# Kernel optimization log

Measured on AMD Instinct MI355X. Metric: run time of the kernel, lower is better.

## Reference

```python
import jax, jax.numpy as jnp
import numpy as np

B, T, C, H = 4, 2048, 1024, 16
D = C // H  # head_dim = 64


def setup_inputs() -> dict:
    key = jax.random.key(0)
    k1, k2, k3 = jax.random.split(key, 3)
    x = jax.random.normal(k1, (B, T, C), dtype=jnp.float32)
    w_attn = jax.random.normal(k2, (C, 3 * C), dtype=jnp.float32) * (1.0 / np.sqrt(C))
    b_attn = jnp.zeros((3 * C,), dtype=jnp.float32)
    w_proj = jax.random.normal(k3, (C, C), dtype=jnp.float32) * (1.0 / np.sqrt(C))
    b_proj = jnp.zeros((C,), dtype=jnp.float32)
    return {"x": x, "w_attn": w_attn, "b_attn": b_attn, "w_proj": w_proj, "b_proj": b_proj}


def reference(x, w_attn, b_attn, w_proj, b_proj):
    Bx, Tx, Cx = x.shape
    qkv = x @ w_attn + b_attn                      # (B, T, 3C)
    q, k, v = jnp.split(qkv, 3, axis=2)
    # (B, T, C) -> (B, H, T, D)
    q = q.reshape(Bx, Tx, H, D).transpose(0, 2, 1, 3)
    k = k.reshape(Bx, Tx, H, D).transpose(0, 2, 1, 3)
    v = v.reshape(Bx, Tx, H, D).transpose(0, 2, 1, 3)
    scores = jnp.einsum('bhqd,bhkd->bhqk', q, k) / jnp.sqrt(jnp.float32(D))
    causal = jnp.tril(jnp.ones((Tx, Tx), dtype=bool))
    scores = jnp.where(causal[None, None], scores, jnp.float32(-jnp.inf))
    probs = jax.nn.softmax(scores, axis=-1)
    out = jnp.einsum('bhqk,bhkd->bhqd', probs, v)  # (B, H, T, D)
    out = out.transpose(0, 2, 1, 3).reshape(Bx, Tx, Cx)
    return out @ w_proj + b_proj
```

## Files before the change

kernel.cpp:

```cpp
#include <hip/hip_runtime.h>

#define AS1 __attribute__((address_space(1)))
#define AS3 __attribute__((address_space(3)))

using bf16x8  = __attribute__((ext_vector_type(8))) __bf16;
using floatx4 = __attribute__((ext_vector_type(4))) float;

#define SCQ 0.18033688f

__device__ inline ushort f2b(float f) {
    __bf16 h = (__bf16)f;
    return __builtin_bit_cast(ushort, h);
}

__device__ inline float fexp2(float x) {
    float r;
    asm("v_exp_f32 %0, %1" : "=v"(r) : "v"(x));
    return r;
}

__device__ inline unsigned cvtpk_bf16(float lo, float hi) {
    unsigned r;
    asm("v_cvt_pk_bf16_f32 %0, %1, %2" : "=v"(r) : "v"(lo), "v"(hi));
    return r;
}
__device__ inline void plswap32(unsigned& a, unsigned& b) {
    asm("v_permlane32_swap_b32 %0, %1" : "+v"(a), "+v"(b));
}
__device__ inline void plswap16(unsigned& a, unsigned& b) {
    asm("v_permlane16_swap_b32 %0, %1" : "+v"(a), "+v"(b));
}

#define BARRIER_A() asm volatile("s_waitcnt lgkmcnt(0)\n\ts_barrier" ::: "memory")
#define BARRIER_B() asm volatile("s_barrier" ::: "memory")

__device__ inline bf16x8 pack_swap(floatx4 ej0, floatx4 ej1) {
    unsigned x0 = cvtpk_bf16(ej0[0], ej0[1]);
    unsigned x1 = cvtpk_bf16(ej0[2], ej0[3]);
    unsigned y0 = cvtpk_bf16(ej1[0], ej1[1]);
    unsigned y1 = cvtpk_bf16(ej1[2], ej1[3]);
    plswap32(x0, y0); plswap16(x0, y0);
    plswap32(x1, y1); plswap16(x1, y1);
    union { unsigned u[4]; bf16x8 v; } ua;
    ua.u[0] = x0; ua.u[1] = x1; ua.u[2] = y0; ua.u[3] = y1;
    return ua.v;
}

__global__ void k_prep(const float* __restrict__ x, ushort* __restrict__ xb,
                       const float* __restrict__ wa, ushort* __restrict__ waT,
                       const float* __restrict__ wp, ushort* __restrict__ wpT)
{
    __shared__ float tile[32][33];
    int blk = blockIdx.x;
    if (blk < 8192) {
        int i = (blk * 256 + threadIdx.x) * 4;
        float4 v = *(const float4*)(x + i);
        ushort4 o;
        o.x = f2b(v.x); o.y = f2b(v.y); o.z = f2b(v.z); o.w = f2b(v.w);
        *(ushort4*)(xb + i) = o;
        return;
    }
    const float* in; ushort* out; int R, Ncol, bx, by; float scale; int scale_cols;
    if (blk < 11264) {
        int idx = blk - 8192;
        in = wa; out = waT; R = 1024; Ncol = 3072;
        bx = idx % 96; by = idx / 96; scale = SCQ; scale_cols = 1024;
    } else {
        int idx = blk - 11264;
        in = wp; out = wpT; R = 1024; Ncol = 1024;
        bx = idx % 32; by = idx / 32; scale = 1.0f; scale_cols = 0;
    }
    int tx = threadIdx.x & 31, ty = threadIdx.x >> 5;
    int c0 = bx * 32, r0 = by * 32;
    for (int i = 0; i < 32; i += 8)
        tile[ty + i][tx] = in[(size_t)(r0 + ty + i) * Ncol + c0 + tx];
    __syncthreads();
    for (int i = 0; i < 32; i += 8) {
        int n = c0 + ty + i;
        float v = tile[tx][ty + i];
        if (n < scale_cols) v *= scale;
        out[(size_t)n * R + r0 + tx] = f2b(v);
    }
}

__device__ inline void xcd_swizzle(int& bx, int& by) {
    int gx = gridDim.x, lin = blockIdx.x + gx * blockIdx.y;
    int nwg = gx * gridDim.y;
    int swz = (lin & 7) * (nwg >> 3) + (lin >> 3);
    bx = swz % gx; by = swz / gx;
}

__global__ __launch_bounds__(256, 4) void k_gemm_bt(
    const ushort* __restrict__ A, const ushort* __restrict__ Bt,
    const float* __restrict__ bias, float* __restrict__ outv,
    int M, int N, int K)
{
    __shared__ __align__(16) ushort As[128 * 64];
    __shared__ __align__(16) ushort Bs[128 * 64];
    int tid = threadIdx.x;
    int bxs, bys; xcd_swizzle(bxs, bys);
    int m0 = bys * 128, n0 = bxs * 128;
    int lane = tid & 63;
    int wm = (tid >> 7) * 64;
    int wn = ((tid >> 6) & 1) * 64;
    int lr = lane & 15, quad = lane >> 4;

    floatx4 acc[4][4] = {};
    const ushort* ags[4]; const ushort* bgs[4]; int sdst[4];
    #pragma unroll
    for (int it = 0; it < 4; ++it) {
        int slot = tid + 256 * it;
        int row = slot >> 3, ch = slot & 7;
        ags[it] = A  + (size_t)(m0 + row) * K + ch * 8;
        bgs[it] = Bt + (size_t)(n0 + row) * K + ch * 8;
        sdst[it] = slot * 8;
    }

    for (int kt = 0; kt < K; kt += 64) {
        #pragma unroll
        for (int it = 0; it < 4; ++it) {
            __builtin_amdgcn_global_load_lds((const AS1 unsigned int*)(ags[it] + kt),
                                             (AS3 unsigned int*)&As[sdst[it]], 16, 0, 0);
            __builtin_amdgcn_global_load_lds((const AS1 unsigned int*)(bgs[it] + kt),
                                             (AS3 unsigned int*)&Bs[sdst[it]], 16, 0, 0);
        }
        asm volatile("s_waitcnt vmcnt(0)" ::: "memory");
        __syncthreads();
        bf16x8 af[4][2], bf[4][2];
        #pragma unroll
        for (int i = 0; i < 4; ++i) {
            af[i][0] = *(const bf16x8*)&As[(wm + 16 * i + lr) * 64 + quad * 8];
            af[i][1] = *(const bf16x8*)&As[(wm + 16 * i + lr) * 64 + 32 + quad * 8];
        }
        #pragma unroll
        for (int j = 0; j < 4; ++j) {
            bf[j][0] = *(const bf16x8*)&Bs[(wn + 16 * j + lr) * 64 + quad * 8];
            bf[j][1] = *(const bf16x8*)&Bs[(wn + 16 * j + lr) * 64 + 32 + quad * 8];
        }
        #pragma unroll
        for (int i = 0; i < 4; ++i)
            #pragma unroll
            for (int j = 0; j < 4; ++j) {
                acc[i][j] = __builtin_amdgcn_mfma_f32_16x16x32_bf16(af[i][0], bf[j][0], acc[i][j], 0, 0, 0);
                acc[i][j] = __builtin_amdgcn_mfma_f32_16x16x32_bf16(af[i][1], bf[j][1], acc[i][j], 0, 0, 0);
            }
        __syncthreads();
    }

    #pragma unroll
    for (int j = 0; j < 4; ++j) {
        int col = n0 + wn + 16 * j + lr;
        float bv = bias[col];
        #pragma unroll
        for (int i = 0; i < 4; ++i) {
            int row = m0 + wm + 16 * i + quad * 4;
            #pragma unroll
            for (int r = 0; r < 4; ++r)
                outv[(size_t)(row + r) * N + col] = acc[i][j][r] + bv;
        }
    }
}

__global__ __launch_bounds__(256, 4) void k_gemm_qkv(
    const ushort* __restrict__ A, const ushort* __restrict__ Bt,
    const float* __restrict__ bias, ushort* __restrict__ qkv, ushort* __restrict__ vt)
{
    constexpr int K = 1024;
    __shared__ __align__(16) ushort As[128 * 64];
    __shared__ __align__(16) ushort Bs[128 * 64];
    int tid = threadIdx.x;
    int bxs, bys; xcd_swizzle(bxs, bys);
    int m0 = bys * 128, n0 = bxs * 128;
    int lane = tid & 63;
    int wm = (tid >> 7) * 64;
    int wn = ((tid >> 6) & 1) * 64;
    int lr = lane & 15, quad = lane >> 4;

    floatx4 acc[4][4] = {};
    const ushort* ags[4]; const ushort* bgs[4]; int sdst[4];
    #pragma unroll
    for (int it = 0; it < 4; ++it) {
        int slot = tid + 256 * it;
        int row = slot >> 3, ch = slot & 7;
        ags[it] = A  + (size_t)(m0 + row) * K + ch * 8;
        bgs[it] = Bt + (size_t)(n0 + row) * K + ch * 8;
        sdst[it] = slot * 8;
    }

    for (int kt = 0; kt < K; kt += 64) {
        #pragma unroll
        for (int it = 0; it < 4; ++it) {
            __builtin_amdgcn_global_load_lds((const AS1 unsigned int*)(ags[it] + kt),
                                             (AS3 unsigned int*)&As[sdst[it]], 16, 0, 0);
            __builtin_amdgcn_global_load_lds((const AS1 unsigned int*)(bgs[it] + kt),
                                             (AS3 unsigned int*)&Bs[sdst[it]], 16, 0, 0);
        }
        asm volatile("s_waitcnt vmcnt(0)" ::: "memory");
        __syncthreads();
        bf16x8 af[4][2], bf[4][2];
        #pragma unroll
        for (int i = 0; i < 4; ++i) {
            af[i][0] = *(const bf16x8*)&As[(wm + 16 * i + lr) * 64 + quad * 8];
            af[i][1] = *(const bf16x8*)&As[(wm + 16 * i + lr) * 64 + 32 + quad * 8];
        }
        #pragma unroll
        for (int j = 0; j < 4; ++j) {
            bf[j][0] = *(const bf16x8*)&Bs[(wn + 16 * j + lr) * 64 + quad * 8];
            bf[j][1] = *(const bf16x8*)&Bs[(wn + 16 * j + lr) * 64 + 32 + quad * 8];
        }
        #pragma unroll
        for (int i = 0; i < 4; ++i)
            #pragma unroll
            for (int j = 0; j < 4; ++j) {
                acc[i][j] = __builtin_amdgcn_mfma_f32_16x16x32_bf16(af[i][0], bf[j][0], acc[i][j], 0, 0, 0);
                acc[i][j] = __builtin_amdgcn_mfma_f32_16x16x32_bf16(af[i][1], bf[j][1], acc[i][j], 0, 0, 0);
            }
        __syncthreads();
    }

    int bb = m0 >> 11;
    #pragma unroll
    for (int j = 0; j < 4; ++j) {
        int col = n0 + wn + 16 * j + lr;
        float bv = bias[col];
        if (col < 1024) bv *= SCQ;
        if (col < 2048) {
            #pragma unroll
            for (int i = 0; i < 4; ++i) {
                int row = m0 + wm + 16 * i + quad * 4;
                #pragma unroll
                for (int r = 0; r < 4; ++r)
                    qkv[(size_t)(row + r) * 2048 + col] = f2b(acc[i][j][r] + bv);
            }
        } else {
            int h = (col - 2048) >> 6, d = (col - 2048) & 63;
            ushort* vbase = vt + ((size_t)(bb * 16 + h) * 64 + d) * 2048;
            #pragma unroll
            for (int i = 0; i < 4; ++i) {
                int t0 = (m0 + wm + 16 * i + quad * 4) & 2047;
                ushort4 pk;
                ((ushort*)&pk)[0] = f2b(acc[i][j][0] + bv);
                ((ushort*)&pk)[1] = f2b(acc[i][j][1] + bv);
                ((ushort*)&pk)[2] = f2b(acc[i][j][2] + bv);
                ((ushort*)&pk)[3] = f2b(acc[i][j][3] + bv);
                *(ushort4*)&vbase[t0] = pk;
            }
        }
    }
}

__device__ __forceinline__ void attn_tile(
    const ushort* __restrict__ Kb, const ushort* __restrict__ Vb,
    bf16x8 aq0, bf16x8 aq1, bf16x8 ones,
    floatx4 (&o)[4], floatx4& lacc,
    int kt, int ktd, int qrow, int lr, int quad, int c0, int c1)
{
    floatx4 s[4];
    __builtin_amdgcn_s_setprio(1);
    #pragma unroll
    for (int j = 0; j < 4; ++j) {
        const ushort* kr = &Kb[(16 * j + lr) * 64];
        bf16x8 bk0 = *(const bf16x8*)(kr + c0);
        bf16x8 bk1 = *(const bf16x8*)(kr + c1);
        floatx4 z = {};
        s[j] = __builtin_amdgcn_mfma_f32_16x16x32_bf16(bk0, aq0, z, 0, 0, 0);
        s[j] = __builtin_amdgcn_mfma_f32_16x16x32_bf16(bk1, aq1, s[j], 0, 0, 0);
    }
    __builtin_amdgcn_s_setprio(0);
    floatx4 e[4];
    if (kt == ktd) {
        int qa = qrow + lr;
        #pragma unroll
        for (int j = 0; j < 4; ++j)
            #pragma unroll
            for (int r = 0; r < 4; ++r)
                e[j][r] = ((kt * 64 + 16 * j + quad * 4 + r) > qa) ? 0.f : fexp2(s[j][r]);
    } else {
        #pragma unroll
        for (int j = 0; j < 4; ++j)
            #pragma unroll
            for (int r = 0; r < 4; ++r)
                e[j][r] = fexp2(s[j][r]);
    }
    bf16x8 ap0 = pack_swap(e[0], e[1]);
    bf16x8 ap1 = pack_swap(e[2], e[3]);
    __builtin_amdgcn_s_setprio(1);
    lacc = __builtin_amdgcn_mfma_f32_16x16x32_bf16(ap0, ones, lacc, 0, 0, 0);
    lacc = __builtin_amdgcn_mfma_f32_16x16x32_bf16(ap1, ones, lacc, 0, 0, 0);
    #pragma unroll
    for (int jd = 0; jd < 4; ++jd) {
        const ushort* vr = &Vb[(16 * jd + lr) * 64];
        bf16x8 bv0 = *(const bf16x8*)(vr + c0);
        bf16x8 bv1 = *(const bf16x8*)(vr + c1);
        o[jd] = __builtin_amdgcn_mfma_f32_16x16x32_bf16(ap0, bv0, o[jd], 0, 0, 0);
        o[jd] = __builtin_amdgcn_mfma_f32_16x16x32_bf16(ap1, bv1, o[jd], 0, 0, 0);
    }
    __builtin_amdgcn_s_setprio(0);
}

__global__ __launch_bounds__(512, 4) void k_attn(const ushort* __restrict__ qkv,
                                                 const ushort* __restrict__ vt,
                                                 ushort* __restrict__ out)
{
    constexpr int T = 2048, SQK = 2048, C = 1024;
    __shared__ __align__(16) ushort Ks[4][64 * 64];
    __shared__ __align__(16) ushort Vs[4][64 * 64];
    int tid = threadIdx.x;
    int lane = tid & 63, wave = tid >> 6;
    int lr = lane & 15, quad = lane >> 4, lk = quad * 8;

    int lin = blockIdx.x + 8 * blockIdx.y;
    int qt  = lin >> 6;
    int bh  = lin & 63;
    int b = bh >> 4, h = bh & 15;
    size_t base = (size_t)b * T * SQK;
    const ushort* kg0 = qkv + base + 1024 + h * 64;
    const ushort* vg0 = vt + (size_t)bh * 64 * 2048;

    int srow = tid >> 3;
    int sg   = (tid & 7) ^ (srow & 7);
    int sdst = tid * 8;
    const ushort* kgs = kg0 + (size_t)srow * SQK + sg * 8;
    const ushort* vgs = vg0 + (size_t)srow * 2048 + sg * 8;

    bf16x8 ones;
    #pragma unroll
    for (int i = 0; i < 8; ++i) ones[i] = (__bf16)1.0f;
    int c0 = (quad ^ (lr & 7)) * 8;
    int c1 = ((4 + quad) ^ (lr & 7)) * 8;

    int qtA = qt, qtB = 15 - qt;
    int qrowA = qtA * 128 + wave * 16;
    int qrowB = qtB * 128 + wave * 16;
    int ktdA = qrowA >> 6, ktdB = qrowB >> 6;
    const ushort* qpA = qkv + base + (size_t)(qrowA + lr) * SQK + h * 64;
    const ushort* qpB = qkv + base + (size_t)(qrowB + lr) * SQK + h * 64;
    bf16x8 aqA0 = *(const bf16x8*)(qpA + lk);
    bf16x8 aqA1 = *(const bf16x8*)(qpA + 32 + lk);
    bf16x8 aqB0 = *(const bf16x8*)(qpB + lk);
    bf16x8 aqB1 = *(const bf16x8*)(qpB + 32 + lk);
    floatx4 oA[4] = {}, oB[4] = {};
    floatx4 laccA = {}, laccB = {};
    int ktmax = 2 * qtB + 1;

    #pragma unroll
    for (int p = 0; p < 3; ++p) {
        __builtin_amdgcn_global_load_lds((const AS1 unsigned int*)(kgs + (size_t)p * 64 * SQK),
                                         (AS3 unsigned int*)&Ks[p][sdst], 16, 0, 0);
        __builtin_amdgcn_global_load_lds((const AS1 unsigned int*)(vgs + p * 64),
                                         (AS3 unsigned int*)&Vs[p][sdst], 16, 0, 0);
    }

    for (int kt = 0; kt <= ktmax; ++kt) {
        BARRIER_A();
        if (kt + 3 <= ktmax) {
            int bidx = (kt + 3) & 3;
            __builtin_amdgcn_global_load_lds((const AS1 unsigned int*)(kgs + (size_t)(kt + 3) * 64 * SQK),
                                             (AS3 unsigned int*)&Ks[bidx][sdst], 16, 0, 0);
            __builtin_amdgcn_global_load_lds((const AS1 unsigned int*)(vgs + (kt + 3) * 64),
                                             (AS3 unsigned int*)&Vs[bidx][sdst], 16, 0, 0);
            asm volatile("s_waitcnt vmcnt(6)" ::: "memory");
        } else if (kt + 2 <= ktmax) {
            asm volatile("s_waitcnt vmcnt(4)" ::: "memory");
        } else if (kt + 1 <= ktmax) {
            asm volatile("s_waitcnt vmcnt(2)" ::: "memory");
        } else {
            asm volatile("s_waitcnt vmcnt(0)" ::: "memory");
        }
        BARRIER_B();

        const ushort* Kb = Ks[kt & 3];
        const ushort* Vb = Vs[kt & 3];
        if (kt <= ktdB)
            attn_tile(Kb, Vb, aqB0, aqB1, ones, oB, laccB, kt, ktdB, qrowB, lr, quad, c0, c1);
        if (kt <= ktdA)
            attn_tile(Kb, Vb, aqA0, aqA1, ones, oA, laccA, kt, ktdA, qrowA, lr, quad, c0, c1);
    }

    #pragma unroll
    for (int r = 0; r < 4; ++r) {
        float invA = 1.0f / laccA[r];
        float invB = 1.0f / laccB[r];
        int rowA = b * T + qrowA + quad * 4 + r;
        int rowB = b * T + qrowB + quad * 4 + r;
        #pragma unroll
        for (int jd = 0; jd < 4; ++jd) {
            out[(size_t)rowA * C + h * 64 + 16 * jd + lr] = f2b(oA[jd][r] * invA);
            out[(size_t)rowB * C + h * 64 + 16 * jd + lr] = f2b(oB[jd][r] * invB);
        }
    }
}

extern "C" void kernel_launch(void* const* d_in, const int* in_sizes, int n_in,
                              void* d_out, int out_size, void* d_ws, size_t ws_size,
                              hipStream_t stream) {
    const float* x      = (const float*)d_in[0];
    const float* w_attn = (const float*)d_in[1];
    const float* b_attn = (const float*)d_in[2];
    const float* w_proj = (const float*)d_in[3];
    const float* b_proj = (const float*)d_in[4];
    float* out = (float*)d_out;

    constexpr int Bb = 4, T = 2048, C = 1024;
    constexpr int M = Bb * T;

    ushort* xb  = (ushort*)d_ws;
    ushort* waT = xb  + (size_t)M * C;
    ushort* wpT = waT + (size_t)3 * C * C;
    ushort* qkv = wpT + (size_t)C * C;
    ushort* vt  = qkv + (size_t)M * 2 * C;
    ushort* ao  = vt  + (size_t)64 * 64 * T;

    k_prep<<<12288, 256, 0, stream>>>(x, xb, w_attn, waT, w_proj, wpT);
    k_gemm_qkv<<<dim3(3 * C / 128, M / 128), 256, 0, stream>>>(xb, waT, b_attn, qkv, vt);
    k_attn<<<dim3(8, Bb * 16), 512, 0, stream>>>(qkv, vt, ao);
    k_gemm_bt<<<dim3(C / 128, M / 128), 256, 0, stream>>>(ao, wpT, b_proj, out, M, C, C);
}
```

Measured before the change: 236.5 us.

## Store K in per-head packed layout and relax GEMM launch bounds

```diff
diff --git a/kernel.cpp b/kernel.cpp
--- a/kernel.cpp
+++ b/kernel.cpp
@@ -90,7 +90,7 @@
     bx = swz % gx; by = swz / gx;
 }
 
-__global__ __launch_bounds__(256, 4) void k_gemm_bt(
+__global__ __launch_bounds__(256, 2) void k_gemm_bt(
     const ushort* __restrict__ A, const ushort* __restrict__ Bt,
     const float* __restrict__ bias, float* __restrict__ outv,
     int M, int N, int K)
@@ -161,9 +161,10 @@
     }
 }
 
-__global__ __launch_bounds__(256, 4) void k_gemm_qkv(
+__global__ __launch_bounds__(256, 2) void k_gemm_qkv(
     const ushort* __restrict__ A, const ushort* __restrict__ Bt,
-    const float* __restrict__ bias, ushort* __restrict__ qkv, ushort* __restrict__ vt)
+    const float* __restrict__ bias, ushort* __restrict__ qb,
+    ushort* __restrict__ kpk, ushort* __restrict__ vt)
 {
     constexpr int K = 1024;
     __shared__ __align__(16) ushort As[128 * 64];
@@ -223,14 +224,24 @@
     for (int j = 0; j < 4; ++j) {
         int col = n0 + wn + 16 * j + lr;
         float bv = bias[col];
-        if (col < 1024) bv *= SCQ;
-        if (col < 2048) {
+        if (col < 1024) {
+            bv *= SCQ;
             #pragma unroll
             for (int i = 0; i < 4; ++i) {
                 int row = m0 + wm + 16 * i + quad * 4;
                 #pragma unroll
                 for (int r = 0; r < 4; ++r)
-                    qkv[(size_t)(row + r) * 2048 + col] = f2b(acc[i][j][r] + bv);
+                    qb[(size_t)(row + r) * 1024 + col] = f2b(acc[i][j][r] + bv);
+            }
+        } else if (col < 2048) {
+            int h = (col - 1024) >> 6, d = (col - 1024) & 63;
+            ushort* kbase = kpk + ((size_t)(bb * 16 + h) * 2048) * 64 + d;
+            #pragma unroll
+            for (int i = 0; i < 4; ++i) {
+                int t0 = (m0 + wm + 16 * i + quad * 4) & 2047;
+                #pragma unroll
+                for (int r = 0; r < 4; ++r)
+                    kbase[(size_t)(t0 + r) * 64] = f2b(acc[i][j][r] + bv);
             }
         } else {
             int h = (col - 2048) >> 6, d = (col - 2048) & 63;
@@ -298,11 +309,12 @@
     __builtin_amdgcn_s_setprio(0);
 }
 
-__global__ __launch_bounds__(512, 4) void k_attn(const ushort* __restrict__ qkv,
+__global__ __launch_bounds__(512, 4) void k_attn(const ushort* __restrict__ qb,
+                                                 const ushort* __restrict__ kpk,
                                                  const ushort* __restrict__ vt,
                                                  ushort* __restrict__ out)
 {
-    constexpr int T = 2048, SQK = 2048, C = 1024;
+    constexpr int T = 2048, C = 1024;
     __shared__ __align__(16) ushort Ks[4][64 * 64];
     __shared__ __align__(16) ushort Vs[4][64 * 64];
     int tid = threadIdx.x;
@@ -313,15 +325,14 @@
     int qt  = lin >> 6;
     int bh  = lin & 63;
     int b = bh >> 4, h = bh & 15;
-    size_t base = (size_t)b * T * SQK;
-    const ushort* kg0 = qkv + base + 1024 + h * 64;
-    const ushort* vg0 = vt + (size_t)bh * 64 * 2048;
+    const ushort* kg0 = kpk + (size_t)bh * T * 64;
+    const ushort* vg0 = vt + (size_t)bh * 64 * T;
 
     int srow = tid >> 3;
     int sg   = (tid & 7) ^ (srow & 7);
     int sdst = tid * 8;
-    const ushort* kgs = kg0 + (size_t)srow * SQK + sg * 8;
-    const ushort* vgs = vg0 + (size_t)srow * 2048 + sg * 8;
+    const ushort* kgs = kg0 + (size_t)srow * 64 + sg * 8;
+    const ushort* vgs = vg0 + (size_t)srow * T + sg * 8;
 
     bf16x8 ones;
     #pragma unroll
@@ -333,8 +344,8 @@
     int qrowA = qtA * 128 + wave * 16;
     int qrowB = qtB * 128 + wave * 16;
     int ktdA = qrowA >> 6, ktdB = qrowB >> 6;
-    const ushort* qpA = qkv + base + (size_t)(qrowA + lr) * SQK + h * 64;
-    const ushort* qpB = qkv + base + (size_t)(qrowB + lr) * SQK + h * 64;
+    const ushort* qpA = qb + ((size_t)(b * T + qrowA + lr)) * 1024 + h * 64;
+    const ushort* qpB = qb + ((size_t)(b * T + qrowB + lr)) * 1024 + h * 64;
     bf16x8 aqA0 = *(const bf16x8*)(qpA + lk);
     bf16x8 aqA1 = *(const bf16x8*)(qpA + 32 + lk);
     bf16x8 aqB0 = *(const bf16x8*)(qpB + lk);
@@ -345,7 +356,7 @@
 
     #pragma unroll
     for (int p = 0; p < 3; ++p) {
-        __builtin_amdgcn_global_load_lds((const AS1 unsigned int*)(kgs + (size_t)p * 64 * SQK),
+        __builtin_amdgcn_global_load_lds((const AS1 unsigned int*)(kgs + (size_t)p * 64 * 64),
                                          (AS3 unsigned int*)&Ks[p][sdst], 16, 0, 0);
         __builtin_amdgcn_global_load_lds((const AS1 unsigned int*)(vgs + p * 64),
                                          (AS3 unsigned int*)&Vs[p][sdst], 16, 0, 0);
@@ -355,7 +366,7 @@
         BARRIER_A();
         if (kt + 3 <= ktmax) {
             int bidx = (kt + 3) & 3;
-            __builtin_amdgcn_global_load_lds((const AS1 unsigned int*)(kgs + (size_t)(kt + 3) * 64 * SQK),
+            __builtin_amdgcn_global_load_lds((const AS1 unsigned int*)(kgs + (size_t)(kt + 3) * 64 * 64),
                                              (AS3 unsigned int*)&Ks[bidx][sdst], 16, 0, 0);
             __builtin_amdgcn_global_load_lds((const AS1 unsigned int*)(vgs + (kt + 3) * 64),
                                              (AS3 unsigned int*)&Vs[bidx][sdst], 16, 0, 0);
@@ -407,12 +418,13 @@
     ushort* xb  = (ushort*)d_ws;
     ushort* waT = xb  + (size_t)M * C;
     ushort* wpT = waT + (size_t)3 * C * C;
-    ushort* qkv = wpT + (size_t)C * C;
-    ushort* vt  = qkv + (size_t)M * 2 * C;
+    ushort* qbf = wpT + (size_t)C * C;
+    ushort* kpk = qbf + (size_t)M * C;
+    ushort* vt  = kpk + (size_t)64 * T * 64;
     ushort* ao  = vt  + (size_t)64 * 64 * T;
 
     k_prep<<<12288, 256, 0, stream>>>(x, xb, w_attn, waT, w_proj, wpT);
-    k_gemm_qkv<<<dim3(3 * C / 128, M / 128), 256, 0, stream>>>(xb, waT, b_attn, qkv, vt);
-    k_attn<<<dim3(8, Bb * 16), 512, 0, stream>>>(qkv, vt, ao);
+    k_gemm_qkv<<<dim3(3 * C / 128, M / 128), 256, 0, stream>>>(xb, waT, b_attn, qbf, kpk, vt);
+    k_attn<<<dim3(8, Bb * 16), 512, 0, stream>>>(qbf, kpk, vt, ao);
     k_gemm_bt<<<dim3(C / 128, M / 128), 256, 0, stream>>>(ao, wpT, b_proj, out, M, C, C);
 }
```

After: 234.6 us, median of 2. No clear change (-0.8%).
